# Kernel optimization log

Measured on AMD Instinct MI355X. Metric: run time of the kernel, lower is better.

## Reference

```python
import jax, jax.numpy as jnp
import numpy as np

N = 100000
E = 1250000
H = 64


def setup_inputs() -> dict:
    key = jax.random.key(0)
    ks = jax.random.split(key, 20)
    x = jax.random.normal(ks[0], (N, 1), dtype=jnp.float32)
    edge_index = jax.random.randint(ks[1], (2, E), 0, N, dtype=jnp.int64)
    edge_attr = jax.random.uniform(ks[2], (E,), dtype=jnp.float32)
    def lin(k, fin, fout):
        s = 1.0 / np.sqrt(fin)
        kw, kb = jax.random.split(k)
        W = jax.random.uniform(kw, (fin, fout), minval=-s, maxval=s, dtype=jnp.float32)
        b = jax.random.uniform(kb, (fout,), minval=-s, maxval=s, dtype=jnp.float32)
        return W, b
    W1, b1 = lin(ks[3], 1, H)
    W2, b2 = lin(ks[4], H, H)
    W3, b3 = lin(ks[5], H, H)
    W4, b4 = lin(ks[6], H, H)
    W5, b5 = lin(ks[7], H, H)
    fW1, fb1 = lin(ks[8], H, H)
    fW2, fb2 = lin(ks[9], H, 1)
    return dict(x=x, edge_index=edge_index, edge_attr=edge_attr,
                W1=W1, b1=b1, W2=W2, b2=b2, W3=W3, b3=b3, W4=W4, b4=b4,
                W5=W5, b5=b5, fW1=fW1, fb1=fb1, fW2=fW2, fb2=fb2)


def _gcn_layer(x, W, b, src, dst, ew):
    # PyG GCNConv: x' = D^{-1/2}(A+I)D^{-1/2} x W + b (self-loops pre-appended)
    h = x @ W                                   # [N, H]
    deg = jax.ops.segment_sum(ew, dst, num_segments=N)
    dinv = jnp.where(deg > 0, jax.lax.rsqrt(deg), 0.0)
    norm = dinv[src] * ew * dinv[dst]           # [E+N]
    msg = h[src] * norm[:, None]                # [E+N, H]
    return jax.ops.segment_sum(msg, dst, num_segments=N) + b


def reference(x, edge_index, edge_attr, W1, b1, W2, b2, W3, b3, W4, b4, W5, b5, fW1, fb1, fW2, fb2):
    loops = jnp.arange(N, dtype=edge_index.dtype)
    src = jnp.concatenate([edge_index[0], loops])
    dst = jnp.concatenate([edge_index[1], loops])
    ew = jnp.concatenate([edge_attr, jnp.ones((N,), edge_attr.dtype)])
    h = jax.nn.relu(_gcn_layer(x, W1, b1, src, dst, ew))
    h = jax.nn.relu(_gcn_layer(h, W2, b2, src, dst, ew))
    h = jax.nn.relu(_gcn_layer(h, W3, b3, src, dst, ew))
    h = jax.nn.relu(_gcn_layer(h, W4, b4, src, dst, ew))
    h = jax.nn.relu(_gcn_layer(h, W5, b5, src, dst, ew))
    h = jax.nn.relu(h @ fW1 + fb1)
    return h @ fW2 + fb2
```

## Files before the change

kernel.cpp:

```cpp
#include <hip/hip_runtime.h>
#include <hip/hip_bf16.h>

#define NN 100000
#define EE 1250000

#define RL(x, l) __builtin_amdgcn_readlane((x), (l))
#define RLF(x, l) __int_as_float(__builtin_amdgcn_readlane(__float_as_int(x), (l)))

typedef __attribute__((ext_vector_type(8))) short v8s;
typedef __attribute__((ext_vector_type(4))) float v4f;
typedef __attribute__((ext_vector_type(4))) unsigned int v4u;

__device__ __forceinline__ unsigned short bf16rtn(float x) {
    unsigned u = __float_as_uint(x);
    unsigned r = u + 0x7fffu + ((u >> 16) & 1u);
    return (unsigned short)(r >> 16);
}
__device__ __forceinline__ unsigned bf16rtn2(float lo, float hi) {
    return (unsigned)bf16rtn(lo) | ((unsigned)bf16rtn(hi) << 16);
}
__device__ __forceinline__ float bflo(unsigned u) { return __uint_as_float(u << 16); }
__device__ __forceinline__ float bfhi(unsigned u) { return __uint_as_float(u & 0xffff0000u); }
__device__ __forceinline__ float bfs(unsigned short s) { return __uint_as_float((unsigned)s << 16); }


__global__ __launch_bounds__(256) void k_count(const int* __restrict__ ei,
                                               const float* __restrict__ ew,
                                               unsigned long long* __restrict__ cnt,
                                               int* __restrict__ slot) {
    int e = blockIdx.x * 256 + threadIdx.x;
    if (e >= EE) return;
    int d = __builtin_nontemporal_load(&ei[EE + e]);
    float w = __builtin_nontemporal_load(&ew[e]);
    unsigned fx = (unsigned)(w * 16777216.0f + 0.5f);
    unsigned long long old =
        atomicAdd(&cnt[d], (1ULL << 32) | (unsigned long long)fx);
    __builtin_nontemporal_store((int)(old >> 32), &slot[e]);
}

__global__ __launch_bounds__(256) void k_bsum(const unsigned long long* __restrict__ cnt,
                                              int* __restrict__ bsum) {
    __shared__ int ls[256];
    int b = blockIdx.x, tid = threadIdx.x;
    int base = b * 1024 + tid * 4;
    int s = 0;
    #pragma unroll
    for (int j = 0; j < 4; ++j) { int g = base + j; if (g < NN) s += (int)(cnt[g] >> 32); }
    ls[tid] = s; __syncthreads();
    for (int off = 128; off > 0; off >>= 1) {
        if (tid < off) ls[tid] += ls[tid + off];
        __syncthreads();
    }
    if (tid == 0) bsum[b] = ls[0];
}

__global__ __launch_bounds__(256) void k_scan_out(const unsigned long long* __restrict__ cnt,
                                                  const int* __restrict__ bsum,
                                                  const float* __restrict__ x,
                                                  int* __restrict__ rowptr,
                                                  float* __restrict__ dinv,
                                                  float* __restrict__ xd) {
    __shared__ int ls[256];
    __shared__ int sbase;
    int b = blockIdx.x, tid = threadIdx.x;
    if (tid < 64) {
        int w0 = (tid < b) ? bsum[tid] : 0;
        int w1 = ((64 + tid) < b) ? bsum[64 + tid] : 0;
        int s = w0 + w1;
        #pragma unroll
        for (int m = 32; m >= 1; m >>= 1) s += __shfl_xor(s, m, 64);
        if (tid == 0) sbase = s;
    }
    int base = b * 1024 + tid * 4;
    int c[4]; float sw[4]; int s = 0;
    #pragma unroll
    for (int j = 0; j < 4; ++j) {
        int g = base + j;
        unsigned long long v = (g < NN) ? cnt[g] : 0ULL;
        c[j] = (int)(v >> 32);
        sw[j] = (float)(unsigned)(v & 0xffffffffu) * (1.0f / 16777216.0f);
        s += c[j];
    }
    ls[tid] = s; __syncthreads();
    for (int off = 1; off < 256; off <<= 1) {
        int v = (tid >= off) ? ls[tid - off] : 0;
        __syncthreads();
        ls[tid] += v;
        __syncthreads();
    }
    int excl = ls[tid] - s + sbase;
    #pragma unroll
    for (int j = 0; j < 4; ++j) {
        int g = base + j;
        if (g < NN) {
            rowptr[g + 1] = excl + c[j];
            excl += c[j];
            float di = rsqrtf(sw[j] + 1.0f);
            dinv[g] = di;
            xd[g] = di * x[g];
        }
    }
    if (b == 0 && tid == 0) rowptr[0] = 0;
}

__global__ __launch_bounds__(256) void k_fill(const int* __restrict__ ei,
                                              const float* __restrict__ ew,
                                              const int* __restrict__ slot,
                                              const int* __restrict__ rowptr,
                                              int2* __restrict__ epair) {
    int e = blockIdx.x * 256 + threadIdx.x;
    if (e >= EE) return;
    int s = __builtin_nontemporal_load(&ei[e]);
    int d = __builtin_nontemporal_load(&ei[EE + e]);
    float w = __builtin_nontemporal_load(&ew[e]);
    int sl = __builtin_nontemporal_load(&slot[e]);
    int p = rowptr[d] + sl;
    epair[p] = make_int2(s, __float_as_int(w));
}

__global__ __launch_bounds__(256) void k_wpk(const float* __restrict__ Wa,
                                             const float* __restrict__ Wb,
                                             const float* __restrict__ Wc,
                                             const float* __restrict__ Wd,
                                             unsigned* __restrict__ Wf) {
    const float* W = (blockIdx.x == 0) ? Wa : (blockIdx.x == 1) ? Wb
                   : (blockIdx.x == 2) ? Wc : Wd;
    unsigned* out = Wf + blockIdx.x * 4096;
    int t = threadIdx.x;
    #pragma unroll
    for (int i = 0; i < 2; ++i) {
        int s = t * 2 + i;
        int lane = s & 63;
        int nt = (s >> 6) & 3;
        int kt = s >> 8;
        int col = nt * 16 + (lane & 15);
        int k0 = kt * 32 + (lane >> 4) * 8;
        unsigned hi[4], lo[4];
        #pragma unroll
        for (int d = 0; d < 4; ++d) {
            float w0 = W[(k0 + 2 * d) * 64 + col];
            float w1 = W[(k0 + 2 * d + 1) * 64 + col];
            unsigned short h0 = bf16rtn(w0), h1 = bf16rtn(w1);
            float r0 = w0 - bfs(h0), r1 = w1 - bfs(h1);
            hi[d] = (unsigned)h0 | ((unsigned)h1 << 16);
            lo[d] = (unsigned)bf16rtn(r0) | ((unsigned)bf16rtn(r1) << 16);
        }
        int gh = (0 * 2 + kt) * 4 + nt;
        int gl = (1 * 2 + kt) * 4 + nt;
        *(v4u*)&out[(gh * 64 + lane) * 4] = (v4u){hi[0], hi[1], hi[2], hi[3]};
        *(v4u*)&out[(gl * 64 + lane) * 4] = (v4u){lo[0], lo[1], lo[2], lo[3]};
    }
}

__device__ __forceinline__ void gatherq8(
    const unsigned* __restrict__ G16, const int2* __restrict__ ep,
    int node, int beg, int end, int l8, float a[8])
{
    uint4 su = *(const uint4*)&G16[node * 32 + l8 * 4];
    a[0] = bflo(su.x); a[1] = bfhi(su.x);
    a[2] = bflo(su.y); a[3] = bfhi(su.y);
    a[4] = bflo(su.z); a[5] = bfhi(su.z);
    a[6] = bflo(su.w); a[7] = bfhi(su.w);
    int j = beg;
    for (; j + 8 <= end; j += 8) {
        uint4 u[8]; float nv[8];
        #pragma unroll
        for (int t = 0; t < 8; ++t) {
            int2 p = ep[j + t];
            nv[t] = __int_as_float(p.y);
            u[t] = *(const uint4*)&G16[p.x * 32 + l8 * 4];
        }
        #pragma unroll
        for (int t = 0; t < 8; ++t) {
            a[0] = fmaf(bflo(u[t].x), nv[t], a[0]);
            a[1] = fmaf(bfhi(u[t].x), nv[t], a[1]);
            a[2] = fmaf(bflo(u[t].y), nv[t], a[2]);
            a[3] = fmaf(bfhi(u[t].y), nv[t], a[3]);
            a[4] = fmaf(bflo(u[t].z), nv[t], a[4]);
            a[5] = fmaf(bfhi(u[t].z), nv[t], a[5]);
            a[6] = fmaf(bflo(u[t].w), nv[t], a[6]);
            a[7] = fmaf(bfhi(u[t].w), nv[t], a[7]);
        }
    }
    if (j < end) {
        uint4 u[8]; float nv[8];
        #pragma unroll
        for (int t = 0; t < 8; ++t) {
            int idx = j + t;
            int2 p = ep[idx < end ? idx : j];
            nv[t] = (idx < end) ? __int_as_float(p.y) : 0.f;
            u[t] = *(const uint4*)&G16[p.x * 32 + l8 * 4];
        }
        #pragma unroll
        for (int t = 0; t < 8; ++t) {
            a[0] = fmaf(bflo(u[t].x), nv[t], a[0]);
            a[1] = fmaf(bfhi(u[t].x), nv[t], a[1]);
            a[2] = fmaf(bflo(u[t].y), nv[t], a[2]);
            a[3] = fmaf(bfhi(u[t].y), nv[t], a[3]);
            a[4] = fmaf(bflo(u[t].z), nv[t], a[4]);
            a[5] = fmaf(bfhi(u[t].z), nv[t], a[5]);
            a[6] = fmaf(bflo(u[t].w), nv[t], a[6]);
            a[7] = fmaf(bfhi(u[t].w), nv[t], a[7]);
        }
    }
}


__global__ __launch_bounds__(256) void k_l1(
    const float* __restrict__ xd, const float* __restrict__ dinv,
    const int* __restrict__ rowptr, const int2* __restrict__ ep,
    const float* __restrict__ W1, const float* __restrict__ b1,
    const float* __restrict__ W2, unsigned short* __restrict__ Gout)
{
    __shared__ float sW[4096];
    int tid = threadIdx.x;
    #pragma unroll
    for (int i = 0; i < 16; ++i) sW[tid + i * 256] = W2[tid + i * 256];
    __syncthreads();
    int lane = tid & 63, l16 = lane & 15, sub = lane >> 4;
    int g4 = blockIdx.x * 4 + (tid >> 6);
    int nodeS = g4 * 4 + sub;
    int beg = rowptr[nodeS], end = rowptr[nodeS + 1];
    float partial = 0.f;
    for (int idx = beg + l16; idx < end; idx += 16) {
        int2 p = ep[idx];
        partial = fmaf(__int_as_float(p.y), xd[p.x], partial);
    }
    #pragma unroll
    for (int m = 8; m >= 1; m >>= 1) partial += __shfl_xor(partial, m, 64);
    float z = dinv[nodeS] * (xd[nodeS] + partial);
    float z0 = RLF(z, 0), z1 = RLF(z, 16), z2 = RLF(z, 32), z3 = RLF(z, 48);
    float w1l = W1[lane], b1l = b1[lane];
    float v0 = fmaxf(fmaf(z0, w1l, b1l), 0.f);
    float v1 = fmaxf(fmaf(z1, w1l, b1l), 0.f);
    float v2 = fmaxf(fmaf(z2, w1l, b1l), 0.f);
    float v3 = fmaxf(fmaf(z3, w1l, b1l), 0.f);
    float a0 = 0.f, a1 = 0.f, a2 = 0.f, a3 = 0.f;
    #pragma unroll
    for (int k = 0; k < 64; ++k) {
        float wk = sW[k * 64 + lane];
        a0 = fmaf(RLF(v0, k), wk, a0);
        a1 = fmaf(RLF(v1, k), wk, a1);
        a2 = fmaf(RLF(v2, k), wk, a2);
        a3 = fmaf(RLF(v3, k), wk, a3);
    }
    int n0 = g4 * 4;
    Gout[(n0 + 0) * 64 + lane] = bf16rtn(dinv[n0 + 0] * a0);
    Gout[(n0 + 1) * 64 + lane] = bf16rtn(dinv[n0 + 1] * a1);
    Gout[(n0 + 2) * 64 + lane] = bf16rtn(dinv[n0 + 2] * a2);
    Gout[(n0 + 3) * 64 + lane] = bf16rtn(dinv[n0 + 3] * a3);
}

__global__ __launch_bounds__(256) void k_gmv(
    const unsigned* __restrict__ G16, const float* __restrict__ dinv,
    const int* __restrict__ rowptr, const int2* __restrict__ ep,
    const float* __restrict__ bias, const unsigned* __restrict__ Wf,
    unsigned short* __restrict__ Gout)
{
    __shared__ __align__(16) unsigned sB[4096];
    __shared__ __align__(16) unsigned sA[4][256];
    int tid = threadIdx.x;
    #pragma unroll
    for (int i = 0; i < 4; ++i)
        ((v4u*)sB)[tid + i * 256] = ((const v4u*)Wf)[tid + i * 256];
    int lane = tid & 63;
    int wid  = tid >> 6;
    int q    = lane >> 3;
    int l8   = lane & 7;
    int n0 = (blockIdx.x * 4 + wid) * 8;
    int node = n0 + q;
    int beg = rowptr[node], end = rowptr[node + 1];
    float a[8];
    gatherq8(G16, ep, node, beg, end, l8, a);
    float din = dinv[node];
    float4 bv0 = ((const float4*)bias)[l8 * 2];
    float4 bv1 = ((const float4*)bias)[l8 * 2 + 1];
    float v0 = fmaxf(fmaf(din, a[0], bv0.x), 0.f);
    float v1 = fmaxf(fmaf(din, a[1], bv0.y), 0.f);
    float v2 = fmaxf(fmaf(din, a[2], bv0.z), 0.f);
    float v3 = fmaxf(fmaf(din, a[3], bv0.w), 0.f);
    float v4 = fmaxf(fmaf(din, a[4], bv1.x), 0.f);
    float v5 = fmaxf(fmaf(din, a[5], bv1.y), 0.f);
    float v6 = fmaxf(fmaf(din, a[6], bv1.z), 0.f);
    float v7 = fmaxf(fmaf(din, a[7], bv1.w), 0.f);
    *(uint4*)&sA[wid][q * 32 + l8 * 4] = make_uint4(
        bf16rtn2(v0, v1), bf16rtn2(v2, v3),
        bf16rtn2(v4, v5), bf16rtn2(v6, v7));
    __syncthreads();
    int rr  = lane & 7;
    int blk = lane >> 4;
    v8s fa0 = *(const v8s*)&sA[wid][rr * 32 +  0 + blk * 4];
    v8s fa1 = *(const v8s*)&sA[wid][rr * 32 + 16 + blk * 4];
    v4f acc[4];
    #pragma unroll
    for (int nt = 0; nt < 4; ++nt) {
        v8s bh0 = *(const v8s*)&sB[((0 * 4 + nt) * 64 + lane) * 4];
        v8s bh1 = *(const v8s*)&sB[((1 * 4 + nt) * 64 + lane) * 4];
        v8s bl0 = *(const v8s*)&sB[((2 * 4 + nt) * 64 + lane) * 4];
        v8s bl1 = *(const v8s*)&sB[((3 * 4 + nt) * 64 + lane) * 4];
        v4f c = {0.f, 0.f, 0.f, 0.f};
        c = __builtin_amdgcn_mfma_f32_16x16x32_bf16(fa0, bl0, c, 0, 0, 0);
        c = __builtin_amdgcn_mfma_f32_16x16x32_bf16(fa1, bl1, c, 0, 0, 0);
        c = __builtin_amdgcn_mfma_f32_16x16x32_bf16(fa0, bh0, c, 0, 0, 0);
        c = __builtin_amdgcn_mfma_f32_16x16x32_bf16(fa1, bh1, c, 0, 0, 0);
        acc[nt] = c;
    }
    int grp = lane >> 4;
    int l16 = lane & 15;
    if (grp < 2) {
        int rb = grp * 4;
        float4 dn = *(const float4*)&dinv[n0 + rb];
        #pragma unroll
        for (int r = 0; r < 4; ++r) {
            float d = (r == 0) ? dn.x : (r == 1) ? dn.y : (r == 2) ? dn.z : dn.w;
            #pragma unroll
            for (int nt = 0; nt < 4; ++nt)
                Gout[(n0 + rb + r) * 64 + nt * 16 + l16] = bf16rtn(d * acc[nt][r]);
        }
    }
}

__global__ __launch_bounds__(256) void k_ghead(
    const unsigned* __restrict__ G16, const float* __restrict__ dinv,
    const int* __restrict__ rowptr, const int2* __restrict__ ep,
    const float* __restrict__ b5, const unsigned* __restrict__ Wf,
    const float* __restrict__ fb1, const float* __restrict__ fW2,
    const float* __restrict__ fb2, float* __restrict__ out)
{
    __shared__ __align__(16) unsigned sB[4096];
    __shared__ __align__(16) unsigned sA[4][256];
    int tid = threadIdx.x;
    #pragma unroll
    for (int i = 0; i < 4; ++i)
        ((v4u*)sB)[tid + i * 256] = ((const v4u*)Wf)[tid + i * 256];
    int lane = tid & 63;
    int wid  = tid >> 6;
    int q    = lane >> 3;
    int l8   = lane & 7;
    int l16  = lane & 15;
    int n0 = (blockIdx.x * 4 + wid) * 8;
    int node = n0 + q;
    float fb1v[4], fw2v[4];
    #pragma unroll
    for (int nt = 0; nt < 4; ++nt) {
        fb1v[nt] = fb1[nt * 16 + l16];
        fw2v[nt] = fW2[nt * 16 + l16];
    }
    float fb2s = fb2[0];
    int beg = rowptr[node], end = rowptr[node + 1];
    float a[8];
    gatherq8(G16, ep, node, beg, end, l8, a);
    float din = dinv[node];
    float4 bv0 = ((const float4*)b5)[l8 * 2];
    float4 bv1 = ((const float4*)b5)[l8 * 2 + 1];
    float v0 = fmaxf(fmaf(din, a[0], bv0.x), 0.f);
    float v1 = fmaxf(fmaf(din, a[1], bv0.y), 0.f);
    float v2 = fmaxf(fmaf(din, a[2], bv0.z), 0.f);
    float v3 = fmaxf(fmaf(din, a[3], bv0.w), 0.f);
    float v4 = fmaxf(fmaf(din, a[4], bv1.x), 0.f);
    float v5 = fmaxf(fmaf(din, a[5], bv1.y), 0.f);
    float v6 = fmaxf(fmaf(din, a[6], bv1.z), 0.f);
    float v7 = fmaxf(fmaf(din, a[7], bv1.w), 0.f);
    *(uint4*)&sA[wid][q * 32 + l8 * 4] = make_uint4(
        bf16rtn2(v0, v1), bf16rtn2(v2, v3),
        bf16rtn2(v4, v5), bf16rtn2(v6, v7));
    __syncthreads();
    int rr  = lane & 7;
    int blk = lane >> 4;
    v8s fa0 = *(const v8s*)&sA[wid][rr * 32 +  0 + blk * 4];
    v8s fa1 = *(const v8s*)&sA[wid][rr * 32 + 16 + blk * 4];
    v4f acc[4];
    #pragma unroll
    for (int nt = 0; nt < 4; ++nt) {
        v8s bh0 = *(const v8s*)&sB[((0 * 4 + nt) * 64 + lane) * 4];
        v8s bh1 = *(const v8s*)&sB[((1 * 4 + nt) * 64 + lane) * 4];
        v8s bl0 = *(const v8s*)&sB[((2 * 4 + nt) * 64 + lane) * 4];
        v8s bl1 = *(const v8s*)&sB[((3 * 4 + nt) * 64 + lane) * 4];
        v4f c = {0.f, 0.f, 0.f, 0.f};
        c = __builtin_amdgcn_mfma_f32_16x16x32_bf16(fa0, bl0, c, 0, 0, 0);
        c = __builtin_amdgcn_mfma_f32_16x16x32_bf16(fa1, bl1, c, 0, 0, 0);
        c = __builtin_amdgcn_mfma_f32_16x16x32_bf16(fa0, bh0, c, 0, 0, 0);
        c = __builtin_amdgcn_mfma_f32_16x16x32_bf16(fa1, bh1, c, 0, 0, 0);
        acc[nt] = c;
    }
    float tr[4];
    #pragma unroll
    for (int r = 0; r < 4; ++r) {
        float t = 0.f;
        #pragma unroll
        for (int nt = 0; nt < 4; ++nt)
            t += fmaxf(acc[nt][r] + fb1v[nt], 0.f) * fw2v[nt];
        #pragma unroll
        for (int m = 8; m >= 1; m >>= 1) t += __shfl_xor(t, m, 64);
        tr[r] = t;
    }
    if (lane == 0) {
        float4 o = {tr[0] + fb2s, tr[1] + fb2s, tr[2] + fb2s, tr[3] + fb2s};
        *(float4*)&out[n0] = o;
    } else if (lane == 16) {
        float4 o = {tr[0] + fb2s, tr[1] + fb2s, tr[2] + fb2s, tr[3] + fb2s};
        *(float4*)&out[n0 + 4] = o;
    }
}


extern "C" void kernel_launch(void* const* d_in, const int* in_sizes, int n_in,
                              void* d_out, int out_size, void* d_ws, size_t ws_size,
                              hipStream_t stream) {
    const float* x   = (const float*)d_in[0];
    const int*   ei  = (const int*)d_in[1];
    const float* ew  = (const float*)d_in[2];
    const float* W1  = (const float*)d_in[3];
    const float* b1  = (const float*)d_in[4];
    const float* W2  = (const float*)d_in[5];
    const float* b2  = (const float*)d_in[6];
    const float* W3  = (const float*)d_in[7];
    const float* b3  = (const float*)d_in[8];
    const float* W4  = (const float*)d_in[9];
    const float* b4  = (const float*)d_in[10];
    const float* W5  = (const float*)d_in[11];
    const float* b5  = (const float*)d_in[12];
    const float* fW1 = (const float*)d_in[13];
    const float* fb1 = (const float*)d_in[14];
    const float* fW2 = (const float*)d_in[15];
    const float* fb2 = (const float*)d_in[16];
    float* out = (float*)d_out;

    char* ws = (char*)d_ws;
    size_t o = 0;
    auto alloc = [&](size_t elems) -> void* {
        void* p = (void*)(ws + o);
        o += ((elems * 4 + 255) / 256) * 256;
        return p;
    };
    float* dinv   = (float*)alloc(NN);
    float* xd     = (float*)alloc(NN);
    int*   rowptr = (int*)alloc(NN + 1);
    unsigned long long* cnt64 = (unsigned long long*)alloc(2 * (size_t)NN);
    int*   bsum   = (int*)alloc(128);
    int2*  epair  = (int2*)alloc(2 * (size_t)EE);
    unsigned* Ga16 = (unsigned*)alloc((size_t)NN * 32);
    unsigned* Gb16 = (unsigned*)alloc((size_t)NN * 32);
    int*   slot   = (int*)alloc(EE);
    unsigned* Wf  = (unsigned*)alloc(4 * 4096);

    int gE  = (EE + 255) / 256;
    int nb  = (NN + 1023) / 1024;
    int gW4 = NN / 16;
    int gW8 = NN / 32;

    k_wpk<<<4, 256, 0, stream>>>(W3, W4, W5, fW1, Wf);
    hipMemsetAsync(cnt64, 0, NN * sizeof(unsigned long long), stream);
    k_count<<<gE, 256, 0, stream>>>(ei, ew, cnt64, slot);
    k_bsum<<<nb, 256, 0, stream>>>(cnt64, bsum);
    k_scan_out<<<nb, 256, 0, stream>>>(cnt64, bsum, x, rowptr, dinv, xd);
    k_fill<<<gE, 256, 0, stream>>>(ei, ew, slot, rowptr, epair);

    k_l1<<<gW4, 256, 0, stream>>>(xd, dinv, rowptr, epair, W1, b1, W2,
                                  (unsigned short*)Ga16);
    k_gmv<<<gW8, 256, 0, stream>>>(Ga16, dinv, rowptr, epair, b2, Wf + 0,
                                   (unsigned short*)Gb16);
    k_gmv<<<gW8, 256, 0, stream>>>(Gb16, dinv, rowptr, epair, b3, Wf + 4096,
                                   (unsigned short*)Ga16);
    k_gmv<<<gW8, 256, 0, stream>>>(Ga16, dinv, rowptr, epair, b4, Wf + 8192,
                                   (unsigned short*)Gb16);
    k_ghead<<<gW8, 256, 0, stream>>>(Gb16, dinv, rowptr, epair, b5, Wf + 12288,
                                     fb1, fW2, fb2, out);
}
```

Measured before the change: 367.0 us.

## Fuse layer-1 scalar aggregation into edge fill via atomics; use MFMA for layer-1 GEMM

The layer-1 scalar neighbour aggregation (w * xd[src]) is now accumulated with float atomics inside the CSR fill kernel. This removes the separate CSR gather pass in k_l1. k_l1 now packs W2 as split bf16 hi/lo fragments and runs the 64x64 transform with MFMA instead of readlane FMA loops, processing 8 nodes per wave. The costs are 1.25M float atomics in k_fill, nondeterministic summation order, and bf16 rounding of layer-1 activations before the matmul.

After: 389.4 us. +6.1%, slower.

```diff
diff --git a/kernel.cpp b/kernel.cpp
--- a/kernel.cpp
+++ b/kernel.cpp
@@ -107,7 +107,9 @@
                                               const float* __restrict__ ew,
                                               const int* __restrict__ slot,
                                               const int* __restrict__ rowptr,
-                                              int2* __restrict__ epair) {
+                                              const float* __restrict__ xd,
+                                              int2* __restrict__ epair,
+                                              float* __restrict__ zacc) {
     int e = blockIdx.x * 256 + threadIdx.x;
     if (e >= EE) return;
     int s = __builtin_nontemporal_load(&ei[e]);
@@ -116,15 +118,17 @@
     int sl = __builtin_nontemporal_load(&slot[e]);
     int p = rowptr[d] + sl;
     epair[p] = make_int2(s, __float_as_int(w));
+    atomicAdd(&zacc[d], w * xd[s]);
 }
 
 __global__ __launch_bounds__(256) void k_wpk(const float* __restrict__ Wa,
                                              const float* __restrict__ Wb,
                                              const float* __restrict__ Wc,
                                              const float* __restrict__ Wd,
+                                             const float* __restrict__ We,
                                              unsigned* __restrict__ Wf) {
     const float* W = (blockIdx.x == 0) ? Wa : (blockIdx.x == 1) ? Wb
-                   : (blockIdx.x == 2) ? Wc : Wd;
+                   : (blockIdx.x == 2) ? Wc : (blockIdx.x == 3) ? Wd : We;
     unsigned* out = Wf + blockIdx.x * 4096;
     int t = threadIdx.x;
     #pragma unroll
@@ -208,47 +212,70 @@
 
 __global__ __launch_bounds__(256) void k_l1(
     const float* __restrict__ xd, const float* __restrict__ dinv,
-    const int* __restrict__ rowptr, const int2* __restrict__ ep,
+    const float* __restrict__ zacc,
     const float* __restrict__ W1, const float* __restrict__ b1,
-    const float* __restrict__ W2, unsigned short* __restrict__ Gout)
+    const unsigned* __restrict__ Wf, unsigned short* __restrict__ Gout)
 {
-    __shared__ float sW[4096];
+    __shared__ __align__(16) unsigned sB[4096];
+    __shared__ __align__(16) unsigned sA[4][256];
     int tid = threadIdx.x;
     #pragma unroll
-    for (int i = 0; i < 16; ++i) sW[tid + i * 256] = W2[tid + i * 256];
+    for (int i = 0; i < 4; ++i)
+        ((v4u*)sB)[tid + i * 256] = ((const v4u*)Wf)[tid + i * 256];
+    int lane = tid & 63;
+    int wid  = tid >> 6;
+    int q    = lane >> 3;
+    int l8   = lane & 7;
+    int n0 = (blockIdx.x * 4 + wid) * 8;
+    int node = n0 + q;
+    float z = dinv[node] * (xd[node] + zacc[node]);
+    float4 wa = ((const float4*)W1)[l8 * 2];
+    float4 wb = ((const float4*)W1)[l8 * 2 + 1];
+    float4 ba = ((const float4*)b1)[l8 * 2];
+    float4 bb = ((const float4*)b1)[l8 * 2 + 1];
+    float v0 = fmaxf(fmaf(z, wa.x, ba.x), 0.f);
+    float v1 = fmaxf(fmaf(z, wa.y, ba.y), 0.f);
+    float v2 = fmaxf(fmaf(z, wa.z, ba.z), 0.f);
+    float v3 = fmaxf(fmaf(z, wa.w, ba.w), 0.f);
+    float v4 = fmaxf(fmaf(z, wb.x, bb.x), 0.f);
+    float v5 = fmaxf(fmaf(z, wb.y, bb.y), 0.f);
+    float v6 = fmaxf(fmaf(z, wb.z, bb.z), 0.f);
+    float v7 = fmaxf(fmaf(z, wb.w, bb.w), 0.f);
+    *(uint4*)&sA[wid][q * 32 + l8 * 4] = make_uint4(
+        bf16rtn2(v0, v1), bf16rtn2(v2, v3),
+        bf16rtn2(v4, v5), bf16rtn2(v6, v7));
     __syncthreads();
-    int lane = tid & 63, l16 = lane & 15, sub = lane >> 4;
-    int g4 = blockIdx.x * 4 + (tid >> 6);
-    int nodeS = g4 * 4 + sub;
-    int beg = rowptr[nodeS], end = rowptr[nodeS + 1];
-    float partial = 0.f;
-    for (int idx = beg + l16; idx < end; idx += 16) {
-        int2 p = ep[idx];
-        partial = fmaf(__int_as_float(p.y), xd[p.x], partial);
-    }
-    #pragma unroll
-    for (int m = 8; m >= 1; m >>= 1) partial += __shfl_xor(partial, m, 64);
-    float z = dinv[nodeS] * (xd[nodeS] + partial);
-    float z0 = RLF(z, 0), z1 = RLF(z, 16), z2 = RLF(z, 32), z3 = RLF(z, 48);
-    float w1l = W1[lane], b1l = b1[lane];
-    float v0 = fmaxf(fmaf(z0, w1l, b1l), 0.f);
-    float v1 = fmaxf(fmaf(z1, w1l, b1l), 0.f);
-    float v2 = fmaxf(fmaf(z2, w1l, b1l), 0.f);
-    float v3 = fmaxf(fmaf(z3, w1l, b1l), 0.f);
-    float a0 = 0.f, a1 = 0.f, a2 = 0.f, a3 = 0.f;
-    #pragma unroll
-    for (int k = 0; k < 64; ++k) {
-        float wk = sW[k * 64 + lane];
-        a0 = fmaf(RLF(v0, k), wk, a0);
-        a1 = fmaf(RLF(v1, k), wk, a1);
-        a2 = fmaf(RLF(v2, k), wk, a2);
-        a3 = fmaf(RLF(v3, k), wk, a3);
-    }
-    int n0 = g4 * 4;
-    Gout[(n0 + 0) * 64 + lane] = bf16rtn(dinv[n0 + 0] * a0);
-    Gout[(n0 + 1) * 64 + lane] = bf16rtn(dinv[n0 + 1] * a1);
-    Gout[(n0 + 2) * 64 + lane] = bf16rtn(dinv[n0 + 2] * a2);
-    Gout[(n0 + 3) * 64 + lane] = bf16rtn(dinv[n0 + 3] * a3);
+    int rr  = lane & 7;
+    int blk = lane >> 4;
+    v8s fa0 = *(const v8s*)&sA[wid][rr * 32 +  0 + blk * 4];
+    v8s fa1 = *(const v8s*)&sA[wid][rr * 32 + 16 + blk * 4];
+    v4f acc[4];
+    #pragma unroll
+    for (int nt = 0; nt < 4; ++nt) {
+        v8s bh0 = *(const v8s*)&sB[((0 * 4 + nt) * 64 + lane) * 4];
+        v8s bh1 = *(const v8s*)&sB[((1 * 4 + nt) * 64 + lane) * 4];
+        v8s bl0 = *(const v8s*)&sB[((2 * 4 + nt) * 64 + lane) * 4];
+        v8s bl1 = *(const v8s*)&sB[((3 * 4 + nt) * 64 + lane) * 4];
+        v4f c = {0.f, 0.f, 0.f, 0.f};
+        c = __builtin_amdgcn_mfma_f32_16x16x32_bf16(fa0, bl0, c, 0, 0, 0);
+        c = __builtin_amdgcn_mfma_f32_16x16x32_bf16(fa1, bl1, c, 0, 0, 0);
+        c = __builtin_amdgcn_mfma_f32_16x16x32_bf16(fa0, bh0, c, 0, 0, 0);
+        c = __builtin_amdgcn_mfma_f32_16x16x32_bf16(fa1, bh1, c, 0, 0, 0);
+        acc[nt] = c;
+    }
+    int grp = lane >> 4;
+    int l16 = lane & 15;
+    if (grp < 2) {
+        int rb = grp * 4;
+        float4 dn = *(const float4*)&dinv[n0 + rb];
+        #pragma unroll
+        for (int r = 0; r < 4; ++r) {
+            float d = (r == 0) ? dn.x : (r == 1) ? dn.y : (r == 2) ? dn.z : dn.w;
+            #pragma unroll
+            for (int nt = 0; nt < 4; ++nt)
+                Gout[(n0 + rb + r) * 64 + nt * 16 + l16] = bf16rtn(d * acc[nt][r]);
+        }
+    }
 }
 
 __global__ __launch_bounds__(256) void k_gmv(
@@ -437,33 +464,34 @@
     float* xd     = (float*)alloc(NN);
     int*   rowptr = (int*)alloc(NN + 1);
     unsigned long long* cnt64 = (unsigned long long*)alloc(2 * (size_t)NN);
+    float* zacc   = (float*)alloc(NN);
     int*   bsum   = (int*)alloc(128);
     int2*  epair  = (int2*)alloc(2 * (size_t)EE);
     unsigned* Ga16 = (unsigned*)alloc((size_t)NN * 32);
     unsigned* Gb16 = (unsigned*)alloc((size_t)NN * 32);
     int*   slot   = (int*)alloc(EE);
-    unsigned* Wf  = (unsigned*)alloc(4 * 4096);
+    unsigned* Wf  = (unsigned*)alloc(5 * 4096);
 
     int gE  = (EE + 255) / 256;
     int nb  = (NN + 1023) / 1024;
-    int gW4 = NN / 16;
     int gW8 = NN / 32;
 
-    k_wpk<<<4, 256, 0, stream>>>(W3, W4, W5, fW1, Wf);
-    hipMemsetAsync(cnt64, 0, NN * sizeof(unsigned long long), stream);
+    k_wpk<<<5, 256, 0, stream>>>(W2, W3, W4, W5, fW1, Wf);
+    hipMemsetAsync(cnt64, 0, NN * sizeof(unsigned long long) + NN * sizeof(float),
+                   stream);
     k_count<<<gE, 256, 0, stream>>>(ei, ew, cnt64, slot);
     k_bsum<<<nb, 256, 0, stream>>>(cnt64, bsum);
     k_scan_out<<<nb, 256, 0, stream>>>(cnt64, bsum, x, rowptr, dinv, xd);
-    k_fill<<<gE, 256, 0, stream>>>(ei, ew, slot, rowptr, epair);
-
-    k_l1<<<gW4, 256, 0, stream>>>(xd, dinv, rowptr, epair, W1, b1, W2,
+    k_fill<<<gE, 256, 0, stream>>>(ei, ew, slot, rowptr, xd, epair, zacc);
+
+    k_l1<<<gW8, 256, 0, stream>>>(xd, dinv, zacc, W1, b1, Wf + 0,
                                   (unsigned short*)Ga16);
-    k_gmv<<<gW8, 256, 0, stream>>>(Ga16, dinv, rowptr, epair, b2, Wf + 0,
+    k_gmv<<<gW8, 256, 0, stream>>>(Ga16, dinv, rowptr, epair, b2, Wf + 4096,
                                    (unsigned short*)Gb16);
-    k_gmv<<<gW8, 256, 0, stream>>>(Gb16, dinv, rowptr, epair, b3, Wf + 4096,
+    k_gmv<<<gW8, 256, 0, stream>>>(Gb16, dinv, rowptr, epair, b3, Wf + 8192,
                                    (unsigned short*)Ga16);
-    k_gmv<<<gW8, 256, 0, stream>>>(Ga16, dinv, rowptr, epair, b4, Wf + 8192,
+    k_gmv<<<gW8, 256, 0, stream>>>(Ga16, dinv, rowptr, epair, b4, Wf + 12288,
                                    (unsigned short*)Gb16);
-    k_ghead<<<gW8, 256, 0, stream>>>(Gb16, dinv, rowptr, epair, b5, Wf + 12288,
+    k_ghead<<<gW8, 256, 0, stream>>>(Gb16, dinv, rowptr, epair, b5, Wf + 16384,
                                      fb1, fW2, fb2, out);
 }
```

## Split feature gather into four 16-column quarter passes with separate matmul kernels

Applied to the files above, without the earlier changes.

Stores node features in a quarter-major layout (four slabs of 16 bf16 columns) and splits each GCN layer into a gather kernel that aggregates one quarter per block and a separate MFMA matmul kernel. Each quarter slab is a quarter of the full feature table, so the randomly gathered rows are meant to stay in cache during the aggregation. This costs an extra round trip of the aggregated activations through global memory and more kernel launches, and the edge list is read four times per layer. The slot buffer now aliases the new Yq buffer.

New measurement: 467.3 us. +27.3%, slower.

```diff
diff --git a/kernel.cpp b/kernel.cpp
--- a/kernel.cpp
+++ b/kernel.cpp
@@ -152,59 +152,6 @@
     }
 }
 
-__device__ __forceinline__ void gatherq8(
-    const unsigned* __restrict__ G16, const int2* __restrict__ ep,
-    int node, int beg, int end, int l8, float a[8])
-{
-    uint4 su = *(const uint4*)&G16[node * 32 + l8 * 4];
-    a[0] = bflo(su.x); a[1] = bfhi(su.x);
-    a[2] = bflo(su.y); a[3] = bfhi(su.y);
-    a[4] = bflo(su.z); a[5] = bfhi(su.z);
-    a[6] = bflo(su.w); a[7] = bfhi(su.w);
-    int j = beg;
-    for (; j + 8 <= end; j += 8) {
-        uint4 u[8]; float nv[8];
-        #pragma unroll
-        for (int t = 0; t < 8; ++t) {
-            int2 p = ep[j + t];
-            nv[t] = __int_as_float(p.y);
-            u[t] = *(const uint4*)&G16[p.x * 32 + l8 * 4];
-        }
-        #pragma unroll
-        for (int t = 0; t < 8; ++t) {
-            a[0] = fmaf(bflo(u[t].x), nv[t], a[0]);
-            a[1] = fmaf(bfhi(u[t].x), nv[t], a[1]);
-            a[2] = fmaf(bflo(u[t].y), nv[t], a[2]);
-            a[3] = fmaf(bfhi(u[t].y), nv[t], a[3]);
-            a[4] = fmaf(bflo(u[t].z), nv[t], a[4]);
-            a[5] = fmaf(bfhi(u[t].z), nv[t], a[5]);
-            a[6] = fmaf(bflo(u[t].w), nv[t], a[6]);
-            a[7] = fmaf(bfhi(u[t].w), nv[t], a[7]);
-        }
-    }
-    if (j < end) {
-        uint4 u[8]; float nv[8];
-        #pragma unroll
-        for (int t = 0; t < 8; ++t) {
-            int idx = j + t;
-            int2 p = ep[idx < end ? idx : j];
-            nv[t] = (idx < end) ? __int_as_float(p.y) : 0.f;
-            u[t] = *(const uint4*)&G16[p.x * 32 + l8 * 4];
-        }
-        #pragma unroll
-        for (int t = 0; t < 8; ++t) {
-            a[0] = fmaf(bflo(u[t].x), nv[t], a[0]);
-            a[1] = fmaf(bfhi(u[t].x), nv[t], a[1]);
-            a[2] = fmaf(bflo(u[t].y), nv[t], a[2]);
-            a[3] = fmaf(bfhi(u[t].y), nv[t], a[3]);
-            a[4] = fmaf(bflo(u[t].z), nv[t], a[4]);
-            a[5] = fmaf(bfhi(u[t].z), nv[t], a[5]);
-            a[6] = fmaf(bflo(u[t].w), nv[t], a[6]);
-            a[7] = fmaf(bfhi(u[t].w), nv[t], a[7]);
-        }
-    }
-}
-
 
 __global__ __launch_bounds__(256) void k_l1(
     const float* __restrict__ xd, const float* __restrict__ dinv,
@@ -245,17 +192,73 @@
         a3 = fmaf(RLF(v3, k), wk, a3);
     }
     int n0 = g4 * 4;
-    Gout[(n0 + 0) * 64 + lane] = bf16rtn(dinv[n0 + 0] * a0);
-    Gout[(n0 + 1) * 64 + lane] = bf16rtn(dinv[n0 + 1] * a1);
-    Gout[(n0 + 2) * 64 + lane] = bf16rtn(dinv[n0 + 2] * a2);
-    Gout[(n0 + 3) * 64 + lane] = bf16rtn(dinv[n0 + 3] * a3);
-}
-
-__global__ __launch_bounds__(256) void k_gmv(
-    const unsigned* __restrict__ G16, const float* __restrict__ dinv,
+    int qo = (lane >> 4) * (NN * 16) + l16;
+    Gout[qo + (n0 + 0) * 16] = bf16rtn(dinv[n0 + 0] * a0);
+    Gout[qo + (n0 + 1) * 16] = bf16rtn(dinv[n0 + 1] * a1);
+    Gout[qo + (n0 + 2) * 16] = bf16rtn(dinv[n0 + 2] * a2);
+    Gout[qo + (n0 + 3) * 16] = bf16rtn(dinv[n0 + 3] * a3);
+}
+
+__global__ __launch_bounds__(256) void k_gq(
+    const unsigned* __restrict__ Gq, const float* __restrict__ dinv,
     const int* __restrict__ rowptr, const int2* __restrict__ ep,
-    const float* __restrict__ bias, const unsigned* __restrict__ Wf,
-    unsigned short* __restrict__ Gout)
+    const float* __restrict__ bias, unsigned* __restrict__ Yq)
+{
+    int bid = blockIdx.x;
+    int q   = (bid & 7) >> 1;
+    int sub = bid & 1;
+    int chunk = (bid >> 3) * 2 + sub;
+    int node0 = chunk * 32;
+    if (node0 >= NN) return;
+    int tid = threadIdx.x;
+    int lane = tid & 63;
+    int q8 = lane >> 3;
+    int l8 = lane & 7;
+    int node = node0 + (tid >> 6) * 8 + q8;
+    const unsigned* G = Gq + (size_t)q * (NN * 8);
+    int beg = rowptr[node], end = rowptr[node + 1];
+    unsigned su = G[node * 8 + l8];
+    float a0 = bflo(su), a1 = bfhi(su);
+    int j = beg;
+    for (; j + 8 <= end; j += 8) {
+        unsigned u[8]; float nv[8];
+        #pragma unroll
+        for (int t = 0; t < 8; ++t) {
+            int2 p = ep[j + t];
+            nv[t] = __int_as_float(p.y);
+            u[t] = G[p.x * 8 + l8];
+        }
+        #pragma unroll
+        for (int t = 0; t < 8; ++t) {
+            a0 = fmaf(bflo(u[t]), nv[t], a0);
+            a1 = fmaf(bfhi(u[t]), nv[t], a1);
+        }
+    }
+    if (j < end) {
+        unsigned u[8]; float nv[8];
+        #pragma unroll
+        for (int t = 0; t < 8; ++t) {
+            int idx = j + t;
+            int2 p = ep[idx < end ? idx : j];
+            nv[t] = (idx < end) ? __int_as_float(p.y) : 0.f;
+            u[t] = G[p.x * 8 + l8];
+        }
+        #pragma unroll
+        for (int t = 0; t < 8; ++t) {
+            a0 = fmaf(bflo(u[t]), nv[t], a0);
+            a1 = fmaf(bfhi(u[t]), nv[t], a1);
+        }
+    }
+    float din = dinv[node];
+    float2 bq = ((const float2*)bias)[q * 8 + l8];
+    float v0 = fmaxf(fmaf(din, a0, bq.x), 0.f);
+    float v1 = fmaxf(fmaf(din, a1, bq.y), 0.f);
+    Yq[(size_t)q * (NN * 8) + node * 8 + l8] = bf16rtn2(v0, v1);
+}
+
+__global__ __launch_bounds__(256) void k_mv2(
+    const unsigned* __restrict__ Yq, const float* __restrict__ dinv,
+    const unsigned* __restrict__ Wf, unsigned short* __restrict__ Gout)
 {
     __shared__ __align__(16) unsigned sB[4096];
     __shared__ __align__(16) unsigned sA[4][256];
@@ -265,27 +268,13 @@
         ((v4u*)sB)[tid + i * 256] = ((const v4u*)Wf)[tid + i * 256];
     int lane = tid & 63;
     int wid  = tid >> 6;
-    int q    = lane >> 3;
+    int q8   = lane >> 3;
     int l8   = lane & 7;
     int n0 = (blockIdx.x * 4 + wid) * 8;
-    int node = n0 + q;
-    int beg = rowptr[node], end = rowptr[node + 1];
-    float a[8];
-    gatherq8(G16, ep, node, beg, end, l8, a);
-    float din = dinv[node];
-    float4 bv0 = ((const float4*)bias)[l8 * 2];
-    float4 bv1 = ((const float4*)bias)[l8 * 2 + 1];
-    float v0 = fmaxf(fmaf(din, a[0], bv0.x), 0.f);
-    float v1 = fmaxf(fmaf(din, a[1], bv0.y), 0.f);
-    float v2 = fmaxf(fmaf(din, a[2], bv0.z), 0.f);
-    float v3 = fmaxf(fmaf(din, a[3], bv0.w), 0.f);
-    float v4 = fmaxf(fmaf(din, a[4], bv1.x), 0.f);
-    float v5 = fmaxf(fmaf(din, a[5], bv1.y), 0.f);
-    float v6 = fmaxf(fmaf(din, a[6], bv1.z), 0.f);
-    float v7 = fmaxf(fmaf(din, a[7], bv1.w), 0.f);
-    *(uint4*)&sA[wid][q * 32 + l8 * 4] = make_uint4(
-        bf16rtn2(v0, v1), bf16rtn2(v2, v3),
-        bf16rtn2(v4, v5), bf16rtn2(v6, v7));
+    int node = n0 + q8;
+    #pragma unroll
+    for (int r = 0; r < 4; ++r)
+        sA[wid][q8 * 32 + r * 8 + l8] = Yq[(size_t)r * (NN * 8) + node * 8 + l8];
     __syncthreads();
     int rr  = lane & 7;
     int blk = lane >> 4;
@@ -315,15 +304,14 @@
             float d = (r == 0) ? dn.x : (r == 1) ? dn.y : (r == 2) ? dn.z : dn.w;
             #pragma unroll
             for (int nt = 0; nt < 4; ++nt)
-                Gout[(n0 + rb + r) * 64 + nt * 16 + l16] = bf16rtn(d * acc[nt][r]);
-        }
-    }
-}
-
-__global__ __launch_bounds__(256) void k_ghead(
-    const unsigned* __restrict__ G16, const float* __restrict__ dinv,
-    const int* __restrict__ rowptr, const int2* __restrict__ ep,
-    const float* __restrict__ b5, const unsigned* __restrict__ Wf,
+                Gout[nt * (NN * 16) + (n0 + rb + r) * 16 + l16] =
+                    bf16rtn(d * acc[nt][r]);
+        }
+    }
+}
+
+__global__ __launch_bounds__(256) void k_head2(
+    const unsigned* __restrict__ Yq, const unsigned* __restrict__ Wf,
     const float* __restrict__ fb1, const float* __restrict__ fW2,
     const float* __restrict__ fb2, float* __restrict__ out)
 {
@@ -335,11 +323,11 @@
         ((v4u*)sB)[tid + i * 256] = ((const v4u*)Wf)[tid + i * 256];
     int lane = tid & 63;
     int wid  = tid >> 6;
-    int q    = lane >> 3;
+    int q8   = lane >> 3;
     int l8   = lane & 7;
     int l16  = lane & 15;
     int n0 = (blockIdx.x * 4 + wid) * 8;
-    int node = n0 + q;
+    int node = n0 + q8;
     float fb1v[4], fw2v[4];
     #pragma unroll
     for (int nt = 0; nt < 4; ++nt) {
@@ -347,23 +335,9 @@
         fw2v[nt] = fW2[nt * 16 + l16];
     }
     float fb2s = fb2[0];
-    int beg = rowptr[node], end = rowptr[node + 1];
-    float a[8];
-    gatherq8(G16, ep, node, beg, end, l8, a);
-    float din = dinv[node];
-    float4 bv0 = ((const float4*)b5)[l8 * 2];
-    float4 bv1 = ((const float4*)b5)[l8 * 2 + 1];
-    float v0 = fmaxf(fmaf(din, a[0], bv0.x), 0.f);
-    float v1 = fmaxf(fmaf(din, a[1], bv0.y), 0.f);
-    float v2 = fmaxf(fmaf(din, a[2], bv0.z), 0.f);
-    float v3 = fmaxf(fmaf(din, a[3], bv0.w), 0.f);
-    float v4 = fmaxf(fmaf(din, a[4], bv1.x), 0.f);
-    float v5 = fmaxf(fmaf(din, a[5], bv1.y), 0.f);
-    float v6 = fmaxf(fmaf(din, a[6], bv1.z), 0.f);
-    float v7 = fmaxf(fmaf(din, a[7], bv1.w), 0.f);
-    *(uint4*)&sA[wid][q * 32 + l8 * 4] = make_uint4(
-        bf16rtn2(v0, v1), bf16rtn2(v2, v3),
-        bf16rtn2(v4, v5), bf16rtn2(v6, v7));
+    #pragma unroll
+    for (int r = 0; r < 4; ++r)
+        sA[wid][q8 * 32 + r * 8 + l8] = Yq[(size_t)r * (NN * 8) + node * 8 + l8];
     __syncthreads();
     int rr  = lane & 7;
     int blk = lane >> 4;
@@ -441,13 +415,15 @@
     int2*  epair  = (int2*)alloc(2 * (size_t)EE);
     unsigned* Ga16 = (unsigned*)alloc((size_t)NN * 32);
     unsigned* Gb16 = (unsigned*)alloc((size_t)NN * 32);
-    int*   slot   = (int*)alloc(EE);
+    unsigned* Yq   = (unsigned*)alloc((size_t)NN * 32);
+    int*   slot   = (int*)Yq;
     unsigned* Wf  = (unsigned*)alloc(4 * 4096);
 
     int gE  = (EE + 255) / 256;
     int nb  = (NN + 1023) / 1024;
     int gW4 = NN / 16;
     int gW8 = NN / 32;
+    int gQ  = 8 * 1563;
 
     k_wpk<<<4, 256, 0, stream>>>(W3, W4, W5, fW1, Wf);
     hipMemsetAsync(cnt64, 0, NN * sizeof(unsigned long long), stream);
@@ -458,12 +434,12 @@
 
     k_l1<<<gW4, 256, 0, stream>>>(xd, dinv, rowptr, epair, W1, b1, W2,
                                   (unsigned short*)Ga16);
-    k_gmv<<<gW8, 256, 0, stream>>>(Ga16, dinv, rowptr, epair, b2, Wf + 0,
-                                   (unsigned short*)Gb16);
-    k_gmv<<<gW8, 256, 0, stream>>>(Gb16, dinv, rowptr, epair, b3, Wf + 4096,
-                                   (unsigned short*)Ga16);
-    k_gmv<<<gW8, 256, 0, stream>>>(Ga16, dinv, rowptr, epair, b4, Wf + 8192,
-                                   (unsigned short*)Gb16);
-    k_ghead<<<gW8, 256, 0, stream>>>(Gb16, dinv, rowptr, epair, b5, Wf + 12288,
-                                     fb1, fW2, fb2, out);
-}
+    k_gq<<<gQ, 256, 0, stream>>>(Ga16, dinv, rowptr, epair, b2, Yq);
+    k_mv2<<<gW8, 256, 0, stream>>>(Yq, dinv, Wf + 0, (unsigned short*)Gb16);
+    k_gq<<<gQ, 256, 0, stream>>>(Gb16, dinv, rowptr, epair, b3, Yq);
+    k_mv2<<<gW8, 256, 0, stream>>>(Yq, dinv, Wf + 4096, (unsigned short*)Ga16);
+    k_gq<<<gQ, 256, 0, stream>>>(Ga16, dinv, rowptr, epair, b4, Yq);
+    k_mv2<<<gW8, 256, 0, stream>>>(Yq, dinv, Wf + 8192, (unsigned short*)Gb16);
+    k_gq<<<gQ, 256, 0, stream>>>(Gb16, dinv, rowptr, epair, b5, Yq);
+    k_head2<<<gW8, 256, 0, stream>>>(Yq, Wf + 12288, fb1, fW2, fb2, out);
+}
```
